# Performance work log

Measured on AMD Instinct MI355X. Metric: run time of the kernel, lower is better.

Reference implementation:

```python
import jax, jax.numpy as jnp
import numpy as np

H = 8      # hidden_size
IN = 14    # input_size
B = 4096   # batch
T = 512    # seq_len
BN_EPS = 1e-5


def setup_inputs() -> dict:
    key = jax.random.key(0)
    ks = jax.random.split(key, 16)
    s = lambda k, shape, scale=0.25: jax.random.normal(k, shape, jnp.float32) * scale
    return {
        "x": jax.random.normal(ks[0], (B, T, IN), jnp.float32),
        # layer 1 LSTM params (PyTorch gate order: i, f, g, o)
        "Wih1": s(ks[1], (4 * H, IN)), "Whh1": s(ks[2], (4 * H, H)),
        "bih1": s(ks[3], (4 * H,)), "bhh1": s(ks[4], (4 * H,)),
        # layer 2 LSTM params
        "Wih2": s(ks[5], (4 * H, H)), "Whh2": s(ks[6], (4 * H, H)),
        "bih2": s(ks[7], (4 * H,)), "bhh2": s(ks[8], (4 * H,)),
        # BatchNorm1d(H) params + running stats (eval mode)
        "bn_gamma": jnp.ones((H,), jnp.float32), "bn_beta": jnp.zeros((H,), jnp.float32),
        "bn_mean": s(ks[9], (H,), 0.01), "bn_var": jnp.ones((H,), jnp.float32),
        # MLP head
        "w1": s(ks[10], (4, H)), "b1": s(ks[11], (4,)),
        "w2": s(ks[12], (1, 4)), "b2": s(ks[13], (1,)),
    }


def _cell(gates, c):
    # gates: [B, 4H] pre-activation, PyTorch order i, f, g, o
    i, f, g, o = jnp.split(gates, 4, axis=-1)
    c_new = jax.nn.sigmoid(f) * c + jax.nn.sigmoid(i) * jnp.tanh(g)
    h_new = jax.nn.sigmoid(o) * jnp.tanh(c_new)
    return h_new, c_new


def _lstm_last(x, Wih1, Whh1, bih1, bhh1, Wih2, Whh2, bih2, bhh2):
    # x: [B, T, IN] -> returns last hidden state of layer 2: [B, H]
    xt = jnp.swapaxes(x, 0, 1)  # [T, B, IN]
    # precompute input projections for layer 1 in one big GEMM
    xp1 = jnp.einsum('tbf,gf->tbg', xt, Wih1) + (bih1 + bhh1)  # [T, B, 4H]
    b2sum = bih2 + bhh2
    Bn = x.shape[0]
    z = jnp.zeros((Bn, H), x.dtype)
    init = (z, z, z, z)  # h1, c1, h2, c2

    def step(carry, xp):
        h1, c1, h2, c2 = carry
        h1, c1 = _cell(xp + h1 @ Whh1.T, c1)
        h2, c2 = _cell(h1 @ Wih2.T + h2 @ Whh2.T + b2sum, c2)
        return (h1, c1, h2, c2), None

    (h1, c1, h2, c2), _ = jax.lax.scan(step, init, xp1)
    return h2


def reference(x, Wih1, Whh1, bih1, bhh1, Wih2, Whh2, bih2, bhh2,
              bn_gamma, bn_beta, bn_mean, bn_var, w1, b1, w2, b2):
    last = _lstm_last(x, Wih1, Whh1, bih1, bhh1, Wih2, Whh2, bih2, bhh2)  # [B, H]
    # BatchNorm1d in eval mode (running stats); dropout is identity in eval
    normed = bn_gamma * (last - bn_mean) / jnp.sqrt(bn_var + BN_EPS) + bn_beta
    h = jax.nn.relu(normed @ w1.T + b1)  # [B, 4]
    out = h @ w2.T + b2                  # [B, 1]
    return out.squeeze(-1)               # [B]
```

## Files before the change

kernel.cpp:

```cpp
#include <hip/hip_runtime.h>

#define T_SEQ 512
#define INPUT 14
#define HID 8
#define TC 16
#define NCHUNK (T_SEQ / TC)
#define BN_EPS 1e-5f

typedef float v2f __attribute__((ext_vector_type(2)));

__device__ __forceinline__ float fast_exp2(float x) { return __builtin_amdgcn_exp2f(x); }
__device__ __forceinline__ float fast_rcp(float x)  { return __builtin_amdgcn_rcpf(x); }

__device__ __forceinline__ v2f pk_fma(v2f a, v2f b, v2f c) {
    v2f d;
    asm("v_pk_fma_f32 %0, %1, %2, %3" : "=v"(d) : "v"(a), "v"(b), "v"(c));
    return d;
}
__device__ __forceinline__ v2f pk_mul(v2f a, v2f b) {
    v2f d;
    asm("v_pk_mul_f32 %0, %1, %2" : "=v"(d) : "v"(a), "v"(b));
    return d;
}
__device__ __forceinline__ v2f pk_add(v2f a, v2f b) {
    v2f d;
    asm("v_pk_add_f32 %0, %1, %2" : "=v"(d) : "v"(a), "v"(b));
    return d;
}

template <int IMM>
__device__ __forceinline__ float swz(float v) {
    return __int_as_float(__builtin_amdgcn_ds_swizzle(__float_as_int(v), IMM));
}

#define DPP_BC0  0x00
#define DPP_BC1  0x55
#define DPP_BC2  0xAA
#define DPP_BC3  0xFF
#define DPP_XOR8 0x128
template <int CTRL>
__device__ __forceinline__ float dpp(float v) {
    return __int_as_float(__builtin_amdgcn_update_dpp(
        0, __float_as_int(v), CTRL, 0xF, 0xF, true));
}

__device__ __forceinline__ void butterfly8v(float h, v2f (&hx)[4]) {
    float x8  = dpp<DPP_XOR8>(h);
    float x4  = swz<0x101F>(h);
    float x16 = swz<0x401F>(h);
    float x20 = swz<0x501F>(h);
    hx[0].x = h;   hx[0].y = x8;
    hx[1].x = x4;  hx[1].y = dpp<DPP_XOR8>(x4);
    hx[2].x = x16; hx[2].y = dpp<DPP_XOR8>(x16);
    hx[3].x = x20; hx[3].y = dpp<DPP_XOR8>(x20);
}

__global__ __launch_bounds__(256, 2)
void lstm_forex_kernel(const float* __restrict__ x,
                       const float* __restrict__ Wih1, const float* __restrict__ Whh1,
                       const float* __restrict__ bih1, const float* __restrict__ bhh1,
                       const float* __restrict__ Wih2, const float* __restrict__ Whh2,
                       const float* __restrict__ bih2, const float* __restrict__ bhh2,
                       const float* __restrict__ bn_gamma, const float* __restrict__ bn_beta,
                       const float* __restrict__ bn_mean, const float* __restrict__ bn_var,
                       const float* __restrict__ w1p, const float* __restrict__ b1p,
                       const float* __restrict__ w2p, const float* __restrict__ b2p,
                       float* __restrict__ out)
{
    __shared__ float xbuf[4][2][TC][16];

    const int tid  = threadIdx.x;
    const int wave = tid >> 6;
    const int lane = tid & 63;
    const int grp  = lane >> 5;
    const int l5   = lane & 31;
    const int u    = (l5 >> 2) & 7;
    const int type = l5 & 3;
    const int row  = type * 8 + u;

    const int b = blockIdx.x * 8 + wave * 2 + grp;

    const float gateScale = (type == 2) ? -2.885390082f : -1.4426950408f;
    const float actMul    = (type == 2) ? -5.770780164f : 1.f;
    const float actAdd    = (type == 2) ?  2.885390082f : 0.f;

    v2f wi1p[7], wh1v[4], wi2v[4], wh2v[4];
#pragma unroll
    for (int k = 0; k < 7; ++k) {
        wi1p[k].x = Wih1[row * INPUT + 2 * k]     * gateScale;
        wi1p[k].y = Wih1[row * INPUT + 2 * k + 1] * gateScale;
    }
    const int poff[4] = {0, 1, 4, 5};
#pragma unroll
    for (int p = 0; p < 4; ++p) {
        int j0 = u ^ poff[p], j1 = j0 ^ 2;
        wh1v[p].x = Whh1[row * HID + j0] * gateScale;
        wh1v[p].y = Whh1[row * HID + j1] * gateScale;
        wi2v[p].x = Wih2[row * HID + j0] * gateScale;
        wi2v[p].y = Wih2[row * HID + j1] * gateScale;
        wh2v[p].x = Whh2[row * HID + j0] * gateScale;
        wh2v[p].y = Whh2[row * HID + j1] * gateScale;
    }
    const float bsum1s = (bih1[row] + bhh1[row]) * gateScale;
    const float bsum2s = (bih2[row] + bhh2[row]) * gateScale;
    const v2f   bias1  = { bsum1s, 0.f };
    const v2f   bias2  = { bsum2s, 0.f };

    const float* gptr[7];
    int loff[7];
#pragma unroll
    for (int it = 0; it < 7; ++it) {
        int d   = it * 64 + lane;
        int es  = d / 224;
        int idx = d - es * 224;
        int tr  = idx / 14;
        int k   = idx - tr * 14;
        int bb  = blockIdx.x * 8 + wave * 2 + es;
        gptr[it] = x + (size_t)bb * (T_SEQ * INPUT) + idx;
        loff[it] = es * (TC * 16) + tr * 16 + k;
    }

    v2f hx1[4], hx2[4];
    float c1 = 0.f, c2 = 0.f;
#pragma unroll
    for (int p = 0; p < 4; ++p) { hx1[p] = (v2f){0.f, 0.f}; hx2[p] = (v2f){0.f, 0.f}; }

    float st[7];
#pragma unroll
    for (int it = 0; it < 7; ++it) { st[it] = *gptr[it]; gptr[it] += TC * INPUT; }

    float (*xw)[TC][16] = xbuf[wave];

    for (int c = 0; c < NCHUNK; ++c) {
#pragma unroll
        for (int it = 0; it < 7; ++it) ((float*)xw)[loff[it]] = st[it];
        if (c + 1 < NCHUNK) {
#pragma unroll
            for (int it = 0; it < 7; ++it) { st[it] = *gptr[it]; gptr[it] += TC * INPUT; }
        }
        __builtin_amdgcn_wave_barrier();

        v2f xp0[TC], xp1[TC];
#pragma unroll
        for (int t = 0; t < TC; ++t) {
            const float* xrow = &xw[grp][t][0];
            float4 xa = *(const float4*)(xrow + 0);
            float4 xb = *(const float4*)(xrow + 4);
            float4 xc = *(const float4*)(xrow + 8);
            float2 xd = *(const float2*)(xrow + 12);
            v2f a0 = pk_fma((v2f){xa.x, xa.y}, wi1p[0], bias1);
            v2f a1 = pk_mul((v2f){xa.z, xa.w}, wi1p[1]);
            a0 = pk_fma((v2f){xb.x, xb.y}, wi1p[2], a0);
            a1 = pk_fma((v2f){xb.z, xb.w}, wi1p[3], a1);
            a0 = pk_fma((v2f){xc.x, xc.y}, wi1p[4], a0);
            a1 = pk_fma((v2f){xc.z, xc.w}, wi1p[5], a1);
            a0 = pk_fma((v2f){xd.x, xd.y}, wi1p[6], a0);
            xp0[t] = a0;
            xp1[t] = a1;
        }

#pragma unroll
        for (int t = 0; t < TC; ++t) {
            v2f qA = pk_fma(hx2[0], wh2v[0], bias2);
            v2f qB = pk_mul(hx2[1], wh2v[1]);
            qA = pk_fma(hx2[2], wh2v[2], qA);
            qB = pk_fma(hx2[3], wh2v[3], qB);

            v2f sA = pk_fma(hx1[0], wh1v[0], xp0[t]);
            v2f sB = pk_fma(hx1[1], wh1v[1], xp1[t]);
            sA = pk_fma(hx1[2], wh1v[2], sA);
            sB = pk_fma(hx1[3], wh1v[3], sB);
            v2f sC = pk_add(sA, sB);
            float acc = sC.x + sC.y;

            float v0 = fmaf(fast_rcp(1.f + fast_exp2(acc)), actMul, actAdd);
            float vi = dpp<DPP_BC0>(v0);
            float vf = dpp<DPP_BC1>(v0);
            float vg = dpp<DPP_BC2>(v0);
            float vo = dpp<DPP_BC3>(v0);
            c1 = fmaf(vf, c1, vi * vg);
            float th1 = fmaf(fast_rcp(1.f + fast_exp2(c1)), 2.f, -1.f);
            float h1u = vo * th1;
            butterfly8v(h1u, hx1);

            v2f pA = pk_fma(hx1[0], wi2v[0], qA);
            v2f pB = pk_fma(hx1[1], wi2v[1], qB);
            pA = pk_fma(hx1[2], wi2v[2], pA);
            pB = pk_fma(hx1[3], wi2v[3], pB);
            v2f pC = pk_add(pA, pB);
            float acc2 = pC.x + pC.y;

            float u0 = fmaf(fast_rcp(1.f + fast_exp2(acc2)), actMul, actAdd);
            float ui = dpp<DPP_BC0>(u0);
            float uf = dpp<DPP_BC1>(u0);
            float ug = dpp<DPP_BC2>(u0);
            float uo = dpp<DPP_BC3>(u0);
            c2 = fmaf(uf, c2, ui * ug);
            float th2 = fmaf(fast_rcp(1.f + fast_exp2(c2)), 2.f, -1.f);
            float h2u = uo * th2;
            butterfly8v(h2u, hx2);
        }
    }

    if (l5 == 0) {
        float h2v[HID];
        h2v[0] = hx2[0].x; h2v[2] = hx2[0].y;
        h2v[1] = hx2[1].x; h2v[3] = hx2[1].y;
        h2v[4] = hx2[2].x; h2v[6] = hx2[2].y;
        h2v[5] = hx2[3].x; h2v[7] = hx2[3].y;
        float nd[HID];
#pragma unroll
        for (int j = 0; j < HID; ++j) {
            float inv = 1.f / sqrtf(bn_var[j] + BN_EPS);
            nd[j] = bn_gamma[j] * (h2v[j] - bn_mean[j]) * inv + bn_beta[j];
        }
        float acc = b2p[0];
#pragma unroll
        for (int m = 0; m < 4; ++m) {
            float s = b1p[m];
#pragma unroll
            for (int j = 0; j < HID; ++j) s = fmaf(nd[j], w1p[m * HID + j], s);
            s = fmaxf(s, 0.f);
            acc = fmaf(s, w2p[m], acc);
        }
        out[b] = acc;
    }
}

extern "C" void kernel_launch(void* const* d_in, const int* in_sizes, int n_in,
                              void* d_out, int out_size, void* d_ws, size_t ws_size,
                              hipStream_t stream) {
    const float* x        = (const float*)d_in[0];
    const float* Wih1     = (const float*)d_in[1];
    const float* Whh1     = (const float*)d_in[2];
    const float* bih1     = (const float*)d_in[3];
    const float* bhh1     = (const float*)d_in[4];
    const float* Wih2     = (const float*)d_in[5];
    const float* Whh2     = (const float*)d_in[6];
    const float* bih2     = (const float*)d_in[7];
    const float* bhh2     = (const float*)d_in[8];
    const float* bn_gamma = (const float*)d_in[9];
    const float* bn_beta  = (const float*)d_in[10];
    const float* bn_mean  = (const float*)d_in[11];
    const float* bn_var   = (const float*)d_in[12];
    const float* w1p      = (const float*)d_in[13];
    const float* b1p      = (const float*)d_in[14];
    const float* w2p      = (const float*)d_in[15];
    const float* b2p      = (const float*)d_in[16];
    float* out = (float*)d_out;

    const int B = in_sizes[0] / (T_SEQ * INPUT);
    dim3 grid(B / 8), block(256);
    hipLaunchKernelGGL(lstm_forex_kernel, grid, block, 0, stream,
                       x, Wih1, Whh1, bih1, bhh1, Wih2, Whh2, bih2, bhh2,
                       bn_gamma, bn_beta, bn_mean, bn_var, w1p, b1p, w2p, b2p, out);
}
```

Measured before the change: 315.4 us.

## Wavefront-pipeline the two LSTM layers across wave halves, one sequence per wave

```diff
diff --git a/kernel.cpp b/kernel.cpp
--- a/kernel.cpp
+++ b/kernel.cpp
@@ -15,11 +15,6 @@
 __device__ __forceinline__ v2f pk_fma(v2f a, v2f b, v2f c) {
     v2f d;
     asm("v_pk_fma_f32 %0, %1, %2, %3" : "=v"(d) : "v"(a), "v"(b), "v"(c));
-    return d;
-}
-__device__ __forceinline__ v2f pk_mul(v2f a, v2f b) {
-    v2f d;
-    asm("v_pk_mul_f32 %0, %1, %2" : "=v"(d) : "v"(a), "v"(b));
     return d;
 }
 __device__ __forceinline__ v2f pk_add(v2f a, v2f b) {
@@ -55,7 +50,7 @@
     hx[3].x = x20; hx[3].y = dpp<DPP_XOR8>(x20);
 }
 
-__global__ __launch_bounds__(256, 2)
+__global__ __launch_bounds__(256, 4)
 void lstm_forex_kernel(const float* __restrict__ x,
                        const float* __restrict__ Wih1, const float* __restrict__ Whh1,
                        const float* __restrict__ bih1, const float* __restrict__ bhh1,
@@ -67,110 +62,104 @@
                        const float* __restrict__ w2p, const float* __restrict__ b2p,
                        float* __restrict__ out)
 {
-    __shared__ float xbuf[4][2][TC][16];
+    __shared__ float xbuf[4][TC][16];
 
     const int tid  = threadIdx.x;
     const int wave = tid >> 6;
     const int lane = tid & 63;
-    const int grp  = lane >> 5;
+    const int half = lane >> 5;
     const int l5   = lane & 31;
     const int u    = (l5 >> 2) & 7;
     const int type = l5 & 3;
     const int row  = type * 8 + u;
 
-    const int b = blockIdx.x * 8 + wave * 2 + grp;
+    const int b = blockIdx.x * 4 + wave;
 
     const float gateScale = (type == 2) ? -2.885390082f : -1.4426950408f;
     const float actMul    = (type == 2) ? -5.770780164f : 1.f;
     const float actAdd    = (type == 2) ?  2.885390082f : 0.f;
 
-    v2f wi1p[7], wh1v[4], wi2v[4], wh2v[4];
+    const float xScale = half ? 0.f : gateScale;
+    const float bScale = half ? gateScale : 0.f;
+    const float* WA    = half ? Whh2 : Whh1;
+
+    v2f wi1p[7], wAv[4], wBv[4];
 #pragma unroll
     for (int k = 0; k < 7; ++k) {
-        wi1p[k].x = Wih1[row * INPUT + 2 * k]     * gateScale;
-        wi1p[k].y = Wih1[row * INPUT + 2 * k + 1] * gateScale;
+        wi1p[k].x = Wih1[row * INPUT + 2 * k]     * xScale;
+        wi1p[k].y = Wih1[row * INPUT + 2 * k + 1] * xScale;
     }
     const int poff[4] = {0, 1, 4, 5};
 #pragma unroll
     for (int p = 0; p < 4; ++p) {
         int j0 = u ^ poff[p], j1 = j0 ^ 2;
-        wh1v[p].x = Whh1[row * HID + j0] * gateScale;
-        wh1v[p].y = Whh1[row * HID + j1] * gateScale;
-        wi2v[p].x = Wih2[row * HID + j0] * gateScale;
-        wi2v[p].y = Wih2[row * HID + j1] * gateScale;
-        wh2v[p].x = Whh2[row * HID + j0] * gateScale;
-        wh2v[p].y = Whh2[row * HID + j1] * gateScale;
-    }
-    const float bsum1s = (bih1[row] + bhh1[row]) * gateScale;
-    const float bsum2s = (bih2[row] + bhh2[row]) * gateScale;
-    const v2f   bias1  = { bsum1s, 0.f };
-    const v2f   bias2  = { bsum2s, 0.f };
-
-    const float* gptr[7];
-    int loff[7];
-#pragma unroll
-    for (int it = 0; it < 7; ++it) {
-        int d   = it * 64 + lane;
-        int es  = d / 224;
-        int idx = d - es * 224;
-        int tr  = idx / 14;
-        int k   = idx - tr * 14;
-        int bb  = blockIdx.x * 8 + wave * 2 + es;
-        gptr[it] = x + (size_t)bb * (T_SEQ * INPUT) + idx;
-        loff[it] = es * (TC * 16) + tr * 16 + k;
-    }
-
-    v2f hx1[4], hx2[4];
-    float c1 = 0.f, c2 = 0.f;
-#pragma unroll
-    for (int p = 0; p < 4; ++p) { hx1[p] = (v2f){0.f, 0.f}; hx2[p] = (v2f){0.f, 0.f}; }
-
-    float st[7];
-#pragma unroll
-    for (int it = 0; it < 7; ++it) { st[it] = *gptr[it]; gptr[it] += TC * INPUT; }
-
-    float (*xw)[TC][16] = xbuf[wave];
+        wAv[p].x = WA[row * HID + j0] * gateScale;
+        wAv[p].y = WA[row * HID + j1] * gateScale;
+        wBv[p].x = Wih2[row * HID + j0] * bScale;
+        wBv[p].y = Wih2[row * HID + j1] * bScale;
+    }
+    const float bs = (half ? (bih2[row] + bhh2[row]) : (bih1[row] + bhh1[row])) * gateScale;
+    const v2f biasv = { bs, 0.f };
+
+    const float* gptr[4];
+    int loff[4];
+#pragma unroll
+    for (int it = 0; it < 4; ++it) {
+        int d  = it * 64 + lane;
+        int dc = d < 224 ? d : 223;
+        int tr = dc / 14;
+        int k  = dc - tr * 14;
+        gptr[it] = x + (size_t)b * (T_SEQ * INPUT) + dc;
+        loff[it] = tr * 16 + k;
+    }
+    const bool v3 = lane < 32;
+
+    v2f hA[4], vB[4];
+    float cc = 0.f;
+#pragma unroll
+    for (int p = 0; p < 4; ++p) { hA[p] = (v2f){0.f, 0.f}; vB[p] = (v2f){0.f, 0.f}; }
+
+    float st[4];
+#pragma unroll
+    for (int it = 0; it < 4; ++it)
+        if (it < 3 || v3) { st[it] = *gptr[it]; gptr[it] += TC * INPUT; }
+
+    float (*xw)[16] = xbuf[wave];
 
     for (int c = 0; c < NCHUNK; ++c) {
 #pragma unroll
-        for (int it = 0; it < 7; ++it) ((float*)xw)[loff[it]] = st[it];
+        for (int it = 0; it < 4; ++it)
+            if (it < 3 || v3) ((float*)xw)[loff[it]] = st[it];
         if (c + 1 < NCHUNK) {
 #pragma unroll
-            for (int it = 0; it < 7; ++it) { st[it] = *gptr[it]; gptr[it] += TC * INPUT; }
+            for (int it = 0; it < 4; ++it)
+                if (it < 3 || v3) { st[it] = *gptr[it]; gptr[it] += TC * INPUT; }
         }
         __builtin_amdgcn_wave_barrier();
 
-        v2f xp0[TC], xp1[TC];
 #pragma unroll
         for (int t = 0; t < TC; ++t) {
-            const float* xrow = &xw[grp][t][0];
-            float4 xa = *(const float4*)(xrow + 0);
-            float4 xb = *(const float4*)(xrow + 4);
-            float4 xc = *(const float4*)(xrow + 8);
-            float2 xd = *(const float2*)(xrow + 12);
-            v2f a0 = pk_fma((v2f){xa.x, xa.y}, wi1p[0], bias1);
-            v2f a1 = pk_mul((v2f){xa.z, xa.w}, wi1p[1]);
-            a0 = pk_fma((v2f){xb.x, xb.y}, wi1p[2], a0);
-            a1 = pk_fma((v2f){xb.z, xb.w}, wi1p[3], a1);
-            a0 = pk_fma((v2f){xc.x, xc.y}, wi1p[4], a0);
-            a1 = pk_fma((v2f){xc.z, xc.w}, wi1p[5], a1);
-            a0 = pk_fma((v2f){xd.x, xd.y}, wi1p[6], a0);
-            xp0[t] = a0;
-            xp1[t] = a1;
-        }
-
-#pragma unroll
-        for (int t = 0; t < TC; ++t) {
-            v2f qA = pk_fma(hx2[0], wh2v[0], bias2);
-            v2f qB = pk_mul(hx2[1], wh2v[1]);
-            qA = pk_fma(hx2[2], wh2v[2], qA);
-            qB = pk_fma(hx2[3], wh2v[3], qB);
-
-            v2f sA = pk_fma(hx1[0], wh1v[0], xp0[t]);
-            v2f sB = pk_fma(hx1[1], wh1v[1], xp1[t]);
-            sA = pk_fma(hx1[2], wh1v[2], sA);
-            sB = pk_fma(hx1[3], wh1v[3], sB);
-            v2f sC = pk_add(sA, sB);
+            const v2f* xv = (const v2f*)&xw[t][0];
+            v2f x0 = xv[0], x1 = xv[1], x2 = xv[2], x3 = xv[3];
+            v2f x4 = xv[4], x5 = xv[5], x6 = xv[6];
+
+            v2f s0 = pk_fma(x0, wi1p[0], biasv);
+            v2f s1 = pk_fma(x1, wi1p[1], (v2f){0.f, 0.f});
+            s0 = pk_fma(x2, wi1p[2], s0);
+            s1 = pk_fma(x3, wi1p[3], s1);
+            s0 = pk_fma(x4, wi1p[4], s0);
+            s1 = pk_fma(x5, wi1p[5], s1);
+            s0 = pk_fma(x6, wi1p[6], s0);
+
+            s0 = pk_fma(hA[0], wAv[0], s0);
+            s1 = pk_fma(hA[1], wAv[1], s1);
+            s0 = pk_fma(hA[2], wAv[2], s0);
+            s1 = pk_fma(hA[3], wAv[3], s1);
+            s0 = pk_fma(vB[0], wBv[0], s0);
+            s1 = pk_fma(vB[1], wBv[1], s1);
+            s0 = pk_fma(vB[2], wBv[2], s0);
+            s1 = pk_fma(vB[3], wBv[3], s1);
+            v2f sC = pk_add(s0, s1);
             float acc = sC.x + sC.y;
 
             float v0 = fmaf(fast_rcp(1.f + fast_exp2(acc)), actMul, actAdd);
@@ -178,36 +167,57 @@
             float vf = dpp<DPP_BC1>(v0);
             float vg = dpp<DPP_BC2>(v0);
             float vo = dpp<DPP_BC3>(v0);
-            c1 = fmaf(vf, c1, vi * vg);
-            float th1 = fmaf(fast_rcp(1.f + fast_exp2(c1)), 2.f, -1.f);
-            float h1u = vo * th1;
-            butterfly8v(h1u, hx1);
-
-            v2f pA = pk_fma(hx1[0], wi2v[0], qA);
-            v2f pB = pk_fma(hx1[1], wi2v[1], qB);
-            pA = pk_fma(hx1[2], wi2v[2], pA);
-            pB = pk_fma(hx1[3], wi2v[3], pB);
-            v2f pC = pk_add(pA, pB);
-            float acc2 = pC.x + pC.y;
-
-            float u0 = fmaf(fast_rcp(1.f + fast_exp2(acc2)), actMul, actAdd);
-            float ui = dpp<DPP_BC0>(u0);
-            float uf = dpp<DPP_BC1>(u0);
-            float ug = dpp<DPP_BC2>(u0);
-            float uo = dpp<DPP_BC3>(u0);
-            c2 = fmaf(uf, c2, ui * ug);
-            float th2 = fmaf(fast_rcp(1.f + fast_exp2(c2)), 2.f, -1.f);
-            float h2u = uo * th2;
-            butterfly8v(h2u, hx2);
-        }
-    }
-
-    if (l5 == 0) {
+            cc = fmaf(vf, cc, vi * vg);
+            float th = fmaf(fast_rcp(1.f + fast_exp2(cc)), 2.f, -1.f);
+            float hnew = vo * th;
+            butterfly8v(hnew, hA);
+
+            if (c == 0 && t == 0) {
+                if (half) {
+#pragma unroll
+                    for (int p = 0; p < 4; ++p) hA[p] = (v2f){0.f, 0.f};
+                    cc = 0.f;
+                }
+            }
+
+#pragma unroll
+            for (int p = 0; p < 4; ++p) {
+                vB[p].x = __shfl_xor(hA[p].x, 32);
+                vB[p].y = __shfl_xor(hA[p].y, 32);
+            }
+        }
+    }
+
+    {
+        v2f s0 = biasv, s1 = (v2f){0.f, 0.f};
+        s0 = pk_fma(hA[0], wAv[0], s0);
+        s1 = pk_fma(hA[1], wAv[1], s1);
+        s0 = pk_fma(hA[2], wAv[2], s0);
+        s1 = pk_fma(hA[3], wAv[3], s1);
+        s0 = pk_fma(vB[0], wBv[0], s0);
+        s1 = pk_fma(vB[1], wBv[1], s1);
+        s0 = pk_fma(vB[2], wBv[2], s0);
+        s1 = pk_fma(vB[3], wBv[3], s1);
+        v2f sC = pk_add(s0, s1);
+        float acc = sC.x + sC.y;
+
+        float v0 = fmaf(fast_rcp(1.f + fast_exp2(acc)), actMul, actAdd);
+        float vi = dpp<DPP_BC0>(v0);
+        float vf = dpp<DPP_BC1>(v0);
+        float vg = dpp<DPP_BC2>(v0);
+        float vo = dpp<DPP_BC3>(v0);
+        cc = fmaf(vf, cc, vi * vg);
+        float th = fmaf(fast_rcp(1.f + fast_exp2(cc)), 2.f, -1.f);
+        float hnew = vo * th;
+        butterfly8v(hnew, hA);
+    }
+
+    if (lane == 32) {
         float h2v[HID];
-        h2v[0] = hx2[0].x; h2v[2] = hx2[0].y;
-        h2v[1] = hx2[1].x; h2v[3] = hx2[1].y;
-        h2v[4] = hx2[2].x; h2v[6] = hx2[2].y;
-        h2v[5] = hx2[3].x; h2v[7] = hx2[3].y;
+        h2v[0] = hA[0].x; h2v[2] = hA[0].y;
+        h2v[1] = hA[1].x; h2v[3] = hA[1].y;
+        h2v[4] = hA[2].x; h2v[6] = hA[2].y;
+        h2v[5] = hA[3].x; h2v[7] = hA[3].y;
         float nd[HID];
 #pragma unroll
         for (int j = 0; j < HID; ++j) {
@@ -250,7 +260,7 @@
     float* out = (float*)d_out;
 
     const int B = in_sizes[0] / (T_SEQ * INPUT);
-    dim3 grid(B / 8), block(256);
+    dim3 grid(B / 4), block(256);
     hipLaunchKernelGGL(lstm_forex_kernel, grid, block, 0, stream,
                        x, Wih1, Whh1, bih1, bhh1, Wih2, Whh2, bih2, bhh2,
                        bn_gamma, bn_beta, bn_mean, bn_var, w1p, b1p, w2p, b2p, out);
```

New measurement: 437.8 us. 38.8% more time.

## Skew layer-2 LSTM by one timestep to overlap with layer-1 recurrence

Applied to the files above, without the earlier changes.

```diff
diff --git a/kernel.cpp b/kernel.cpp
--- a/kernel.cpp
+++ b/kernel.cpp
@@ -161,19 +161,27 @@
 
 #pragma unroll
         for (int t = 0; t < TC; ++t) {
-            v2f qA = pk_fma(hx2[0], wh2v[0], bias2);
-            v2f qB = pk_mul(hx2[1], wh2v[1]);
-            qA = pk_fma(hx2[2], wh2v[2], qA);
-            qB = pk_fma(hx2[3], wh2v[3], qB);
-
             v2f sA = pk_fma(hx1[0], wh1v[0], xp0[t]);
             v2f sB = pk_fma(hx1[1], wh1v[1], xp1[t]);
             sA = pk_fma(hx1[2], wh1v[2], sA);
             sB = pk_fma(hx1[3], wh1v[3], sB);
             v2f sC = pk_add(sA, sB);
-            float acc = sC.x + sC.y;
-
-            float v0 = fmaf(fast_rcp(1.f + fast_exp2(acc)), actMul, actAdd);
+            float acc1 = sC.x + sC.y;
+
+            v2f qA = pk_fma(hx2[0], wh2v[0], bias2);
+            v2f qB = pk_mul(hx2[1], wh2v[1]);
+            qA = pk_fma(hx2[2], wh2v[2], qA);
+            qB = pk_fma(hx2[3], wh2v[3], qB);
+            v2f pA = pk_fma(hx1[0], wi2v[0], qA);
+            v2f pB = pk_fma(hx1[1], wi2v[1], qB);
+            pA = pk_fma(hx1[2], wi2v[2], pA);
+            pB = pk_fma(hx1[3], wi2v[3], pB);
+            v2f pC = pk_add(pA, pB);
+            float acc2 = pC.x + pC.y;
+
+            float v0 = fmaf(fast_rcp(1.f + fast_exp2(acc1)), actMul, actAdd);
+            float u0 = fmaf(fast_rcp(1.f + fast_exp2(acc2)), actMul, actAdd);
+
             float vi = dpp<DPP_BC0>(v0);
             float vf = dpp<DPP_BC1>(v0);
             float vg = dpp<DPP_BC2>(v0);
@@ -181,16 +189,7 @@
             c1 = fmaf(vf, c1, vi * vg);
             float th1 = fmaf(fast_rcp(1.f + fast_exp2(c1)), 2.f, -1.f);
             float h1u = vo * th1;
-            butterfly8v(h1u, hx1);
-
-            v2f pA = pk_fma(hx1[0], wi2v[0], qA);
-            v2f pB = pk_fma(hx1[1], wi2v[1], qB);
-            pA = pk_fma(hx1[2], wi2v[2], pA);
-            pB = pk_fma(hx1[3], wi2v[3], pB);
-            v2f pC = pk_add(pA, pB);
-            float acc2 = pC.x + pC.y;
-
-            float u0 = fmaf(fast_rcp(1.f + fast_exp2(acc2)), actMul, actAdd);
+
             float ui = dpp<DPP_BC0>(u0);
             float uf = dpp<DPP_BC1>(u0);
             float ug = dpp<DPP_BC2>(u0);
@@ -198,8 +197,39 @@
             c2 = fmaf(uf, c2, ui * ug);
             float th2 = fmaf(fast_rcp(1.f + fast_exp2(c2)), 2.f, -1.f);
             float h2u = uo * th2;
+
+            butterfly8v(h1u, hx1);
             butterfly8v(h2u, hx2);
-        }
+
+            if (c == 0 && t == 0) {
+#pragma unroll
+                for (int p = 0; p < 4; ++p) hx2[p] = (v2f){0.f, 0.f};
+                c2 = 0.f;
+            }
+        }
+    }
+
+    {
+        v2f qA = pk_fma(hx2[0], wh2v[0], bias2);
+        v2f qB = pk_mul(hx2[1], wh2v[1]);
+        qA = pk_fma(hx2[2], wh2v[2], qA);
+        qB = pk_fma(hx2[3], wh2v[3], qB);
+        v2f pA = pk_fma(hx1[0], wi2v[0], qA);
+        v2f pB = pk_fma(hx1[1], wi2v[1], qB);
+        pA = pk_fma(hx1[2], wi2v[2], pA);
+        pB = pk_fma(hx1[3], wi2v[3], pB);
+        v2f pC = pk_add(pA, pB);
+        float acc2 = pC.x + pC.y;
+
+        float u0 = fmaf(fast_rcp(1.f + fast_exp2(acc2)), actMul, actAdd);
+        float ui = dpp<DPP_BC0>(u0);
+        float uf = dpp<DPP_BC1>(u0);
+        float ug = dpp<DPP_BC2>(u0);
+        float uo = dpp<DPP_BC3>(u0);
+        c2 = fmaf(uf, c2, ui * ug);
+        float th2 = fmaf(fast_rcp(1.f + fast_exp2(c2)), 2.f, -1.f);
+        float h2u = uo * th2;
+        butterfly8v(h2u, hx2);
     }
 
     if (l5 == 0) {
```

New measurement: 311.5 us, median of 2. About the same (-1.3%).
